# Kernel tuning notes

Measured on AMD Instinct MI355X. Metric: run time of the kernel, lower is better.

Reference implementation:

```python
import jax, jax.numpy as jnp
import numpy as np

IN_DIM, DIM, H, L, B, N = 20, 128, 8, 3, 2, 192
DH = DIM // H
EPS = 1e-5


def _conv1d(x, w):
    # x: [b, Cin, n], w: [Cout, Cin, 3], pad=1
    return jax.lax.conv_general_dilated(x, w, (1,), [(1, 1)], dimension_numbers=('NCH', 'OIH', 'NCH'))


def _conv2d(x, w):
    # x: [b, Cin, n, n], w: [Cout, Cin, 3, 3], pad=1
    return jax.lax.conv_general_dilated(x, w, (1, 1), [(1, 1), (1, 1)], dimension_numbers=('NCHW', 'OIHW', 'NCHW'))


def _bn(x, g, b, axes):
    # BatchNorm in training mode (batch statistics, biased variance), channel axis = 1
    m = jnp.mean(x, axes, keepdims=True)
    v = jnp.var(x, axes, keepdims=True)
    sh = [1] * x.ndim
    sh[1] = -1
    return (x - m) / jnp.sqrt(v + EPS) * g.reshape(sh) + b.reshape(sh)


def _ln(x, g, b):
    m = jnp.mean(x, -1, keepdims=True)
    v = jnp.var(x, -1, keepdims=True)
    return (x - m) / jnp.sqrt(v + EPS) * g + b


def _seq2pair(c):
    # c: [b, C, n] -> [b, 2C, n, n]; first C channels constant over j, second C constant over i
    b, C, n = c.shape
    a = jnp.broadcast_to(c[:, :, :, None], (b, C, n, n))
    p = jnp.broadcast_to(c[:, :, None, :], (b, C, n, n))
    return jnp.concatenate([a, p], axis=1)


def _forward(seq, mask, conv1_w, conv2_w, ln_g, ln_b, c1d_w, bn1_g, bn1_b, c2d_w, bn2_g, bn2_b,
             wq_w, wq_b, wk_w, wk_b, wv_w, wv_b, wd_w, wd_b, wl_w, wl_b, fc_w, fc_b):
    b, n, _ = seq.shape
    s = seq.transpose(0, 2, 1)                    # [b, in_dim, n]
    x = _conv1d(s, conv1_w).transpose(0, 2, 1)    # [b, n, dim]
    c = _conv1d(s, conv2_w)                       # [b, dim, n]
    c2 = _seq2pair(c)                             # [b, 2*dim, n, n]
    scale = jnp.sqrt(jnp.asarray(DH, x.dtype))
    m4 = mask[:, None, None, :]                   # [b, 1, 1, n]
    for i in range(L):
        c = jax.nn.relu(_bn(_conv1d(c, c1d_w[i]), bn1_g[i], bn1_b[i], (0, 2)))
        x = _ln(x + c.transpose(0, 2, 1), ln_g[i], ln_b[i])
        c2 = c2 + _seq2pair(c)
        c2 = jax.nn.relu(_bn(_conv2d(c2, c2d_w[i]), bn2_g[i], bn2_b[i], (0, 2, 3)))
        dsym = c2 + c2.transpose(0, 1, 3, 2)      # symmetric pair features [b, 2*dim, n, n]
        gate = jax.nn.sigmoid(jnp.einsum('bcij,hc->bhij', dsym, wd_w[i]) + wd_b[i][None, :, None, None])
        heads = lambda y: y.reshape(b, n, H, DH).transpose(0, 2, 1, 3)
        q = heads(jax.nn.relu(x @ wq_w[i].T + wq_b[i]))
        k = heads(jax.nn.relu(x @ wk_w[i].T + wk_b[i]))
        v = heads(jax.nn.relu(x @ wv_w[i].T + wv_b[i]))
        a = jnp.einsum('bhid,bhjd->bhij', q, k) / scale
        e = jnp.exp(a - jnp.max(a, -1, keepdims=True)) * m4   # hand-rolled masked softmax
        attn = e / (jnp.sum(e, -1, keepdims=True) + 1e-6)
        attn = attn * gate                        # post-softmax multiplicative pair bias
        upd = jnp.einsum('bhij,bhjd->bhid', attn, v).transpose(0, 2, 1, 3).reshape(b, n, DIM)
        x = jax.nn.relu((x + upd) @ wl_w[i].T + wl_b[i])   # dropout = identity (eval)
    return jax.nn.relu(x @ fc_w.T + fc_b)


def setup_inputs():
    key = jax.random.key(0)
    ks = jax.random.split(key, 16)
    rn = lambda k, shape, s=0.05: jax.random.normal(k, shape, jnp.float32) * s
    C2 = 2 * DIM
    return {
        'seq': jax.random.normal(ks[0], (B, N, IN_DIM), jnp.float32),
        'mask': (jax.random.uniform(ks[1], (B, N)) > 0.1).astype(jnp.float32),
        'conv1_w': rn(ks[2], (DIM, IN_DIM, 3)),
        'conv2_w': rn(ks[3], (DIM, IN_DIM, 3)),
        'ln_g': jnp.ones((L, DIM), jnp.float32),
        'ln_b': jnp.zeros((L, DIM), jnp.float32),
        'c1d_w': rn(ks[4], (L, DIM, DIM, 3)),
        'bn1_g': jnp.ones((L, DIM), jnp.float32),
        'bn1_b': jnp.zeros((L, DIM), jnp.float32),
        'c2d_w': rn(ks[5], (L, C2, C2, 3, 3), 0.02),
        'bn2_g': jnp.ones((L, C2), jnp.float32),
        'bn2_b': jnp.zeros((L, C2), jnp.float32),
        'wq_w': rn(ks[6], (L, DIM, DIM)), 'wq_b': jnp.zeros((L, DIM), jnp.float32),
        'wk_w': rn(ks[7], (L, DIM, DIM)), 'wk_b': jnp.zeros((L, DIM), jnp.float32),
        'wv_w': rn(ks[8], (L, DIM, DIM)), 'wv_b': jnp.zeros((L, DIM), jnp.float32),
        'wd_w': rn(ks[9], (L, H, C2)), 'wd_b': jnp.zeros((L, H), jnp.float32),
        'wl_w': rn(ks[10], (L, DIM, DIM)), 'wl_b': jnp.zeros((L, DIM), jnp.float32),
        'fc_w': rn(ks[11], (DIM, DIM)), 'fc_b': jnp.zeros((DIM,), jnp.float32),
    }


def reference(seq, mask, conv1_w, conv2_w, ln_g, ln_b, c1d_w, bn1_g, bn1_b, c2d_w, bn2_g, bn2_b,
              wq_w, wq_b, wk_w, wk_b, wv_w, wv_b, wd_w, wd_b, wl_w, wl_b, fc_w, fc_b):
    return _forward(seq, mask, conv1_w, conv2_w, ln_g, ln_b, c1d_w, bn1_g, bn1_b, c2d_w, bn2_g, bn2_b,
                    wq_w, wq_b, wk_w, wk_b, wv_w, wv_b, wd_w, wd_b, wl_w, wl_b, fc_w, fc_b)
```

## Files before the change

### kernel.cpp

```cpp
#include <hip/hip_runtime.h>
#include <math.h>

#define IN_DIM 20
#define DIM 128
#define HH 8
#define LL 3
#define BB 2
#define NP 192
#define DHH 16
#define C2 256
#define NN (NP*NP)
#define EPS 1e-5f

#define PR 200
#define PC 224

typedef __bf16 bf16x8 __attribute__((ext_vector_type(8)));
typedef float  f32x16 __attribute__((ext_vector_type(16)));

union Pack8 { __bf16 h[8]; uint4 u; };

#define GLOAD16(gp, lp) \
  __builtin_amdgcn_global_load_lds((const __attribute__((address_space(1))) uint4*)(gp), \
                                   (__attribute__((address_space(3))) uint4*)(lp), 16, 0, 0)

__global__ void k_conv_init(const float* __restrict__ seq, const float* __restrict__ w1,
                            const float* __restrict__ w2, float* __restrict__ X,
                            float* __restrict__ Cc) {
  int t = blockIdx.x, b = blockIdx.y, oc = threadIdx.x;
  __shared__ float ss[3][IN_DIM];
  if (threadIdx.x < 3*IN_DIM) {
    int k = threadIdx.x / IN_DIM, ic = threadIdx.x % IN_DIM;
    int tt = t + k - 1;
    ss[k][ic] = (tt >= 0 && tt < NP) ? seq[(b*NP + tt)*IN_DIM + ic] : 0.f;
  }
  __syncthreads();
  float a1 = 0.f, a2 = 0.f;
  #pragma unroll
  for (int ic = 0; ic < IN_DIM; ic++) {
    #pragma unroll
    for (int k = 0; k < 3; k++) {
      float sv = ss[k][ic];
      a1 = fmaf(w1[(oc*IN_DIM + ic)*3 + k], sv, a1);
      a2 = fmaf(w2[(oc*IN_DIM + ic)*3 + k], sv, a2);
    }
  }
  X[(b*NP + t)*DIM + oc] = a1;
  Cc[(b*DIM + oc)*NP + t] = a2;
}

__global__ __launch_bounds__(768)
void k_conv1d_bn_relu(const float* __restrict__ cin, const float* __restrict__ w,
                      const float* __restrict__ g, const float* __restrict__ bb,
                      float* __restrict__ cout) {
  int oc = blockIdx.x;
  int tid = threadIdx.x;
  int t = tid % NP;
  int sub = tid / NP;
  int b = sub & 1, ih = sub >> 1;
  float acc = 0.f;
  for (int ic = ih*64; ic < ih*64 + 64; ic++) {
    const float* cr = cin + (b*DIM + ic)*NP;
    const float* wr = w + (oc*DIM + ic)*3;
    float lf = (t > 0)      ? cr[t-1] : 0.f;
    float mf = cr[t];
    float rf = (t < NP-1)   ? cr[t+1] : 0.f;
    acc = fmaf(lf, wr[0], acc);
    acc = fmaf(mf, wr[1], acc);
    acc = fmaf(rf, wr[2], acc);
  }
  __shared__ float sp[4][NP];
  __shared__ float sb[768];
  sp[sub][t] = acc;
  __syncthreads();
  float raw = sp[b][t] + sp[2 + b][t];
  sb[tid] = (sub < 2) ? raw : raw * raw;
  __syncthreads();
  for (int s = 192; s >= 3; s >>= 1) {
    if (tid < s) sb[tid] += sb[tid + s];
    int u = tid - 384;
    if (u >= 0 && u < s) sb[tid] += sb[tid + s];
    __syncthreads();
  }
  float mean = (sb[0] + sb[1] + sb[2]) / 384.f;
  float var  = (sb[384] + sb[385] + sb[386]) / 384.f - mean*mean;
  float rstd = rsqrtf(var + EPS);
  if (sub < 2)
    cout[(b*DIM + oc)*NP + t] = fmaxf((raw - mean)*rstd*g[oc] + bb[oc], 0.f);
}

__global__ void k_wtrans(const float* __restrict__ wq, const float* __restrict__ wk,
                         const float* __restrict__ wv, const float* __restrict__ wl,
                         const float* __restrict__ fcw,
                         float* __restrict__ wqt, float* __restrict__ wkt,
                         float* __restrict__ wvt, float* __restrict__ wlt,
                         float* __restrict__ fct) {
  int m = blockIdx.y;
  const float* src; float* dst;
  if (m < 3)       { src = wq + (size_t)m*DIM*DIM;     dst = wqt + (size_t)m*DIM*DIM; }
  else if (m < 6)  { src = wk + (size_t)(m-3)*DIM*DIM; dst = wkt + (size_t)(m-3)*DIM*DIM; }
  else if (m < 9)  { src = wv + (size_t)(m-6)*DIM*DIM; dst = wvt + (size_t)(m-6)*DIM*DIM; }
  else if (m < 12) { src = wl + (size_t)(m-9)*DIM*DIM; dst = wlt + (size_t)(m-9)*DIM*DIM; }
  else             { src = fcw;                        dst = fct; }
  int tile = blockIdx.x;
  int ti = tile >> 2, tj = tile & 3;
  int r = threadIdx.x >> 3, c4 = threadIdx.x & 7;
  __shared__ float t[32][33];
  float4 v = *(const float4*)(src + (ti*32 + r)*DIM + tj*32 + c4*4);
  t[r][c4*4+0] = v.x; t[r][c4*4+1] = v.y; t[r][c4*4+2] = v.z; t[r][c4*4+3] = v.w;
  __syncthreads();
  float4 o;
  o.x = t[c4*4+0][r]; o.y = t[c4*4+1][r]; o.z = t[c4*4+2][r]; o.w = t[c4*4+3][r];
  *(float4*)(dst + (tj*32 + r)*DIM + ti*32 + c4*4) = o;
}

__global__ void k_lnqkv(float* __restrict__ X, const float* __restrict__ cc,
                        const float* __restrict__ g, const float* __restrict__ bb,
                        const float* __restrict__ wqt, const float* __restrict__ bq,
                        const float* __restrict__ wkt, const float* __restrict__ bk,
                        const float* __restrict__ wvt, const float* __restrict__ bv,
                        float* __restrict__ Q, float* __restrict__ K, float* __restrict__ V) {
  int t = blockIdx.x, b = blockIdx.y, d = threadIdx.x;
  __shared__ float sb[DIM];
  __shared__ float sy[DIM];
  float v = X[(b*NP + t)*DIM + d] + cc[(b*DIM + d)*NP + t];
  sb[d] = v; __syncthreads();
  for (int s = 64; s > 0; s >>= 1) { if (d < s) sb[d] += sb[d+s]; __syncthreads(); }
  float mean = sb[0] / (float)DIM;
  __syncthreads();
  float dv = v - mean;
  sb[d] = dv*dv; __syncthreads();
  for (int s = 64; s > 0; s >>= 1) { if (d < s) sb[d] += sb[d+s]; __syncthreads(); }
  float var = sb[0] / (float)DIM;
  float rstd = rsqrtf(var + EPS);
  float xn = dv * rstd * g[d] + bb[d];
  X[(b*NP + t)*DIM + d] = xn;
  sy[d] = xn;
  __syncthreads();
  float aq = bq[d], ak = bk[d], av = bv[d];
  for (int e = 0; e < DIM; e++) {
    float xv = sy[e];
    aq = fmaf(wqt[e*DIM + d], xv, aq);
    ak = fmaf(wkt[e*DIM + d], xv, ak);
    av = fmaf(wvt[e*DIM + d], xv, av);
  }
  int h = d >> 4, dh = d & 15;
  size_t o = ((size_t)(b*HH + h)*NP + t)*DHH + dh;
  Q[o] = fmaxf(aq, 0.f); K[o] = fmaxf(ak, 0.f); V[o] = fmaxf(av, 0.f);
}

__global__ void k_wprep(const float* __restrict__ w, __bf16* __restrict__ wtb) {
  int l = blockIdx.x / C2, oc = blockIdx.x % C2;
  int tid = threadIdx.x;
  __shared__ float swt[C2*9];
  const float4* wsrc = (const float4*)(w + ((size_t)(l*C2 + oc))*C2*9);
  for (int idx = tid; idx < 576; idx += 256) ((float4*)swt)[idx] = wsrc[idx];
  __syncthreads();
  for (int v = tid; v < 288; v += 256) {
    int chunk = v / 18, rem = v % 18;
    int kk = rem >> 1, kh = rem & 1;
    Pack8 p;
    #pragma unroll
    for (int e = 0; e < 8; e++)
      p.h[e] = (__bf16)swt[(chunk*16 + kh*8 + e)*9 + kk];
    size_t unit = ((((size_t)(l*16 + chunk)*9 + kk)*2 + kh)*256 + oc);
    ((uint4*)wtb)[unit] = p.u;
  }
}

__global__ void k_make_convin(const float* __restrict__ Cc, const float* __restrict__ CL0,
                              __bf16* __restrict__ inb, float* __restrict__ STATALL) {
  int idx = blockIdx.x*256 + threadIdx.x;
  if (blockIdx.x == 0) {
    for (int z = threadIdx.x; z < 3*2*C2; z += 256) STATALL[z] = 0.f;
  }
  int kh = idx & 1;
  int t = idx >> 1;
  int gcol = t % PC; int t2 = t / PC;
  int grow = t2 % PR; int t3 = t2 / PR;
  int chunk = t3 & 15; int b = t3 >> 4;
  int i = grow - 1, j = gcol - 8;
  Pack8 p;
  if ((unsigned)i < 192u && (unsigned)j < 192u) {
    #pragma unroll
    for (int e = 0; e < 8; e++) {
      int c = chunk*16 + kh*8 + e;
      float v;
      if (c < DIM) v = Cc[(b*DIM + c)*NP + i] + CL0[(b*DIM + c)*NP + i];
      else { int cc = c - DIM; v = Cc[(b*DIM + cc)*NP + j] + CL0[(b*DIM + cc)*NP + j]; }
      p.h[e] = (__bf16)v;
    }
  } else {
    #pragma unroll
    for (int e = 0; e < 8; e++) p.h[e] = (__bf16)0.f;
  }
  ((uint4*)inb)[idx] = p.u;
}

__global__ __launch_bounds__(256, 2)
void k_conv2d_mfma(const __bf16* __restrict__ inb,
                   const __bf16* __restrict__ wtb,
                   __bf16* __restrict__ rawb,
                   float* __restrict__ STAT2) {
  __shared__ __align__(16) uint4 sbuf[2*2176];
  int tid = threadIdx.x;
  int jt = blockIdx.x, it = blockIdx.y, zz = blockIdx.z;
  int b = zz >> 3, oct = zz & 7;
  int i0 = it*8, j0 = jt*64, oc0 = oct*32;
  int lane = tid & 63, wv = tid >> 6;
  int ln31 = lane & 31, khl = lane >> 5;

  const uint4* gW = (const uint4*)wtb;
  const uint4* gI = (const uint4*)inb;

  f32x16 acc[2][2];
  #pragma unroll
  for (int r = 0; r < 2; r++)
    #pragma unroll
    for (int n = 0; n < 2; n++)
      #pragma unroll
      for (int q = 0; q < 16; q++) acc[r][n][q] = 0.f;

  const uint4* gp[9];
  int lofs[9];
  int gstride[9];
  bool gvalid[9];
  #pragma unroll
  for (int t = 0; t < 9; t++) {
    int L = t*4 + wv;
    gvalid[t] = (L < 34);
    if (L < 9) {
      int u = L*64 + lane;
      int kkh = u >> 5;
      int ocl = u & 31;
      gp[t] = gW + (size_t)kkh*256 + oc0 + ocl;
      lofs[t] = u;
      gstride[t] = 4608;
    } else {
      int u = L*64 + lane - 576;
      int r = u / 160;
      int rem = u % 160;
      int kh = rem / 80;
      int c = rem % 80;
      gp[t] = gI + (((size_t)(b*16)*PR) + i0 + r)*PC*2 + (size_t)(j0 + c)*2 + kh;
      lofs[t] = 576 + u;
      gstride[t] = PR*PC*2;
    }
  }

  auto issue = [&](int buf) {
    uint4* lbase = sbuf + buf*2176;
    #pragma unroll
    for (int t = 0; t < 9; t++) {
      if (gvalid[t]) {
        GLOAD16(gp[t], lbase + lofs[t]);
        gp[t] += gstride[t];
      }
    }
  };

  issue(0);

  for (int chunk = 0; chunk < 16; ++chunk) {
    int buf = chunk & 1;
    __syncthreads();
    if (chunk < 15) issue(buf ^ 1);
    const __bf16* Wl = (const __bf16*)(sbuf + buf*2176);
    const __bf16* Il = (const __bf16*)(sbuf + buf*2176 + 576);
    #pragma unroll
    for (int kj = 0; kj < 3; kj++) {
      bf16x8 bfr[4][2];
      #pragma unroll
      for (int rr = 0; rr < 4; rr++) {
        int r = wv*2 + rr;
        #pragma unroll
        for (int ch = 0; ch < 2; ch++) {
          int c = ch*32 + ln31 + kj + 7;
          bfr[rr][ch] = *(const bf16x8*)(Il + ((r*2 + khl)*80 + c)*8);
        }
      }
      #pragma unroll
      for (int ki = 0; ki < 3; ki++) {
        int kk = ki*3 + kj;
        bf16x8 a = *(const bf16x8*)(Wl + ((kk*2 + khl)*32 + ln31)*8);
        #pragma unroll
        for (int row = 0; row < 2; row++)
          #pragma unroll
          for (int ch = 0; ch < 2; ch++)
            acc[row][ch] = __builtin_amdgcn_mfma_f32_32x32x16_bf16(a, bfr[row + ki][ch], acc[row][ch], 0, 0, 0);
      }
    }
  }

  __syncthreads();
  float* trAll = (float*)sbuf;
  float* tr = trAll + wv*(32*33);
  float* sstat = trAll + 4*32*33;
  if (tid < 64) sstat[tid] = 0.f;
  __syncthreads();

  #pragma unroll
  for (int reg = 0; reg < 16; reg++) {
    float v00 = acc[0][0][reg], v01 = acc[0][1][reg];
    float v10 = acc[1][0][reg], v11 = acc[1][1][reg];
    float s = v00 + v01 + v10 + v11;
    float s2 = v00*v00 + v01*v01 + v10*v10 + v11*v11;
    #pragma unroll
    for (int msk = 1; msk <= 16; msk <<= 1) { s += __shfl_xor(s, msk); s2 += __shfl_xor(s2, msk); }
    if (ln31 == 0) {
      int oc_l = (reg & 3) + 8*(reg >> 2) + 4*khl;
      atomicAdd(&sstat[oc_l], s);
      atomicAdd(&sstat[32 + oc_l], s2);
    }
  }

  int Gb = oc0 >> 3;
  uint4* RAWu = (uint4*)rawb;
  #pragma unroll
  for (int row = 0; row < 2; row++) {
    int i = i0 + wv*2 + row;
    #pragma unroll
    for (int ch = 0; ch < 2; ch++) {
      #pragma unroll
      for (int reg = 0; reg < 16; reg++) {
        int r = (reg & 3) + 8*(reg >> 2) + 4*khl;
        tr[r*33 + ln31] = acc[row][ch][reg];
      }
      __builtin_amdgcn_s_waitcnt(0);
      #pragma unroll
      for (int gs = 0; gs < 2; gs++) {
        int g = khl + gs*2;
        Pack8 p;
        #pragma unroll
        for (int e = 0; e < 8; e++) p.h[e] = (__bf16)tr[(g*8 + e)*33 + ln31];
        RAWu[((size_t)(b*32 + Gb + g)*192 + i)*192 + j0 + ch*32 + ln31] = p.u;
      }
      __builtin_amdgcn_s_waitcnt(0);
    }
  }

  __syncthreads();
  if (tid < 32) {
    atomicAdd(&STAT2[oc0 + tid], sstat[tid]);
    atomicAdd(&STAT2[C2 + oc0 + tid], sstat[32 + tid]);
  }
}

template<int WRITE_NEXT>
__global__ __launch_bounds__(384)
void k_bn2_norm_gate(const __bf16* __restrict__ rawb, const float* __restrict__ STAT2,
                     const float* __restrict__ g, const float* __restrict__ bb,
                     const float* __restrict__ wd, const float* __restrict__ CLn,
                     __bf16* __restrict__ inb_next, float* __restrict__ tg) {
  int i = blockIdx.x, b = blockIdx.y;
  int tid = threadIdx.x;
  int j = tid % 192, half = tid / 192;
  __shared__ float sscale[C2], sshift[C2], swd[HH*C2];
  __shared__ float sg[2][HH][192];
  const float inv = 1.f / (float)(BB*NN);
  for (int c = tid; c < C2; c += 384) {
    float mean = STAT2[c] * inv;
    float var  = STAT2[C2 + c] * inv - mean*mean;
    float rstd = rsqrtf(var + EPS);
    float sc = rstd * g[c];
    sscale[c] = sc;
    sshift[c] = bb[c] - mean*sc;
  }
  for (int idx = tid; idx < HH*C2; idx += 384) swd[idx] = wd[idx];
  __syncthreads();
  float gacc[HH] = {};
  const uint4* RAWu = (const uint4*)rawb;
  for (int cu = half*16; cu < half*16 + 16; cu++) {
    Pack8 pr; pr.u = RAWu[((size_t)(b*32 + cu)*NP + i)*NP + j];
    Pack8 p;
    #pragma unroll
    for (int e = 0; e < 8; e++) {
      int c = cu*8 + e;
      float v = (float)pr.h[e];
      v = fmaxf(fmaf(v, sscale[c], sshift[c]), 0.f);
      if (WRITE_NEXT) {
        float nv = v + ((c < DIM) ? CLn[(b*DIM + c)*NP + i] : CLn[(b*DIM + c - DIM)*NP + j]);
        p.h[e] = (__bf16)nv;
      }
      #pragma unroll
      for (int h = 0; h < HH; h++) gacc[h] = fmaf(v, swd[h*C2 + c], gacc[h]);
    }
    if (WRITE_NEXT) {
      size_t unit = ((((size_t)(b*16 + (cu>>1))*PR + (i+1))*PC + (j+8))*2 + (cu&1));
      ((uint4*)inb_next)[unit] = p.u;
    }
  }
  #pragma unroll
  for (int h = 0; h < HH; h++) sg[half][h][j] = gacc[h];
  __syncthreads();
  if (half == 0) {
    #pragma unroll
    for (int h = 0; h < HH; h++)
      tg[((size_t)(b*HH + h)*NP + i)*NP + j] = sg[0][h][j] + sg[1][h][j];
  }
}

__global__ void k_gate(const float* __restrict__ tg, const float* __restrict__ wdb,
                       float* __restrict__ gate) {
  int tile = blockIdx.x;
  int hb = blockIdx.y;
  int b = hb >> 3, h = hb & 7;
  size_t bh = (size_t)(b*HH + h);
  int ti = tile / 6, tj = tile % 6;
  int r = threadIdx.x >> 3, c4 = threadIdx.x & 7;
  __shared__ float tB[32][33];
  const float* base = tg + bh*NN;
  float4 vb = *(const float4*)(base + (tj*32 + r)*NP + ti*32 + c4*4);
  tB[r][c4*4+0] = vb.x; tB[r][c4*4+1] = vb.y; tB[r][c4*4+2] = vb.z; tB[r][c4*4+3] = vb.w;
  __syncthreads();
  float4 va = *(const float4*)(base + (ti*32 + r)*NP + tj*32 + c4*4);
  float bias = wdb[h];
  float4 o;
  o.x = 1.f / (1.f + expf(-(va.x + tB[c4*4+0][r] + bias)));
  o.y = 1.f / (1.f + expf(-(va.y + tB[c4*4+1][r] + bias)));
  o.z = 1.f / (1.f + expf(-(va.z + tB[c4*4+2][r] + bias)));
  o.w = 1.f / (1.f + expf(-(va.w + tB[c4*4+3][r] + bias)));
  *(float4*)(gate + bh*NN + (ti*32 + r)*NP + tj*32 + c4*4) = o;
}

template<int MODE>
__global__ __launch_bounds__(384)
void k_attnx(const float* __restrict__ Q, const float* __restrict__ K,
             const float* __restrict__ V, const float* __restrict__ gate,
             const float* __restrict__ mask,
             float* __restrict__ X,
             const float* __restrict__ wlt, const float* __restrict__ bl,
             const float* __restrict__ ccn,
             const float* __restrict__ lng, const float* __restrict__ lnb,
             const float* __restrict__ wqt, const float* __restrict__ bq,
             const float* __restrict__ wkt, const float* __restrict__ bk,
             const float* __restrict__ wvt, const float* __restrict__ bv,
             float* __restrict__ Qn, float* __restrict__ Kn, float* __restrict__ Vn,
             const float* __restrict__ fct, const float* __restrict__ fb,
             float* __restrict__ out) {
  int i = blockIdx.x, b = blockIdx.y;
  int tid = threadIdx.x;
  int j = tid % 192, half = tid / 192;
  int lane = tid & 63, wave = tid >> 6;
  __shared__ float sq[DIM];
  __shared__ float sattn[HH][NP];
  __shared__ float spv[3][DIM];
  __shared__ float supd[DIM];
  __shared__ float sy[DIM];
  __shared__ float sxp[3][DIM];
  __shared__ float sredm[HH][3];
  __shared__ float sreds[HH][3];
  __shared__ float sred[2];
  float mk = mask[b*NP + j];

  if (tid < DIM) {
    int h = tid >> 4, d = tid & 15;
    sq[tid] = Q[(((size_t)(b*HH + h))*NP + i)*DHH + d];
  }
  __syncthreads();

  float a[4], gt[4];
  #pragma unroll
  for (int hh = 0; hh < 4; hh++) {
    int h = half*4 + hh;
    size_t bh = (size_t)(b*HH + h);
    const float4* kr = (const float4*)(K + (bh*NP + j)*DHH);
    const float4* qr = (const float4*)(sq + h*DHH);
    float acc = 0.f;
    #pragma unroll
    for (int q4 = 0; q4 < 4; q4++) {
      float4 qv = qr[q4], kv = kr[q4];
      acc = fmaf(qv.x, kv.x, acc); acc = fmaf(qv.y, kv.y, acc);
      acc = fmaf(qv.z, kv.z, acc); acc = fmaf(qv.w, kv.w, acc);
    }
    a[hh] = acc * 0.25f;
    gt[hh] = gate[(bh*NP + i)*NP + j];
  }
  #pragma unroll
  for (int hh = 0; hh < 4; hh++) {
    int h = half*4 + hh;
    float m = a[hh];
    #pragma unroll
    for (int s = 32; s > 0; s >>= 1) m = fmaxf(m, __shfl_xor(m, s));
    if (lane == 0) sredm[h][wave % 3] = m;
  }
  __syncthreads();
  float e[4];
  #pragma unroll
  for (int hh = 0; hh < 4; hh++) {
    int h = half*4 + hh;
    float amax = fmaxf(fmaxf(sredm[h][0], sredm[h][1]), sredm[h][2]);
    e[hh] = expf(a[hh] - amax) * mk;
    float ss = e[hh];
    #pragma unroll
    for (int s = 32; s > 0; s >>= 1) ss += __shfl_xor(ss, s);
    if (lane == 0) sreds[h][wave % 3] = ss;
  }
  __syncthreads();
  #pragma unroll
  for (int hh = 0; hh < 4; hh++) {
    int h = half*4 + hh;
    float denom = sreds[h][0] + sreds[h][1] + sreds[h][2] + 1e-6f;
    sattn[h][j] = (e[hh] / denom) * gt[hh];
  }
  __syncthreads();

  {
    int d = tid & 15, h2 = (tid >> 4) & 7, jseg = tid >> 7;
    size_t bh = (size_t)(b*HH + h2);
    float acc = 0.f;
    for (int jj = jseg*64; jj < jseg*64 + 64; jj++)
      acc = fmaf(sattn[h2][jj], V[(bh*NP + jj)*DHH + d], acc);
    spv[jseg][h2*DHH + d] = acc;
  }
  __syncthreads();
  if (tid < DIM) supd[tid] = spv[0][tid] + spv[1][tid] + spv[2][tid];
  __syncthreads();

  size_t o = (size_t)(b*NP + i)*DIM;
  if (tid < DIM) sy[tid] = X[o + tid] + supd[tid];
  __syncthreads();
  {
    int d2 = tid & 127, ks = tid >> 7;
    int e0 = ks*43, e1 = (ks == 2) ? 128 : e0 + 43;
    float acc = (ks == 0) ? bl[d2] : 0.f;
    for (int ee = e0; ee < e1; ee++) acc = fmaf(wlt[ee*DIM + d2], sy[ee], acc);
    sxp[ks][d2] = acc;
  }
  __syncthreads();
  float xr = 0.f;
  if (tid < DIM) xr = fmaxf(sxp[0][tid] + sxp[1][tid] + sxp[2][tid], 0.f);
  __syncthreads();

  if (MODE == 0) {
    float v = 0.f;
    if (tid < DIM) v = xr + ccn[(b*DIM + tid)*NP + i];
    if (tid < DIM) {
      float s = v;
      #pragma unroll
      for (int m = 32; m > 0; m >>= 1) s += __shfl_xor(s, m);
      if (lane == 0) sred[wave] = s;
    }
    __syncthreads();
    float mean = (sred[0] + sred[1]) * (1.f/128.f);
    float dv = v - mean;
    if (tid < DIM) {
      float q = dv*dv;
      #pragma unroll
      for (int m = 32; m > 0; m >>= 1) q += __shfl_xor(q, m);
      if (lane == 0) sred[wave] = q;
    }
    __syncthreads();
    float var = (sred[0] + sred[1]) * (1.f/128.f);
    float rstd = rsqrtf(var + EPS);
    if (tid < DIM) {
      float xn = dv * rstd * lng[tid] + lnb[tid];
      X[o + tid] = xn;
      sy[tid] = xn;
    }
    __syncthreads();
    {
      int d2 = tid & 127, m = tid >> 7;
      const float* wt_m = (m == 0) ? wqt : (m == 1) ? wkt : wvt;
      const float* b_m  = (m == 0) ? bq  : (m == 1) ? bk  : bv;
      float* out_m      = (m == 0) ? Qn  : (m == 1) ? Kn  : Vn;
      float acc = b_m[d2];
      for (int ee = 0; ee < DIM; ee++) acc = fmaf(wt_m[ee*DIM + d2], sy[ee], acc);
      int h = d2 >> 4, dh = d2 & 15;
      out_m[((size_t)(b*HH + h)*NP + i)*DHH + dh] = fmaxf(acc, 0.f);
    }
  } else {
    if (tid < DIM) sy[tid] = xr;
    __syncthreads();
    {
      int d2 = tid & 127, ks = tid >> 7;
      int e0 = ks*43, e1 = (ks == 2) ? 128 : e0 + 43;
      float acc = (ks == 0) ? fb[d2] : 0.f;
      for (int ee = e0; ee < e1; ee++) acc = fmaf(fct[ee*DIM + d2], sy[ee], acc);
      sxp[ks][d2] = acc;
    }
    __syncthreads();
    if (tid < DIM)
      out[o + tid] = fmaxf(sxp[0][tid] + sxp[1][tid] + sxp[2][tid], 0.f);
  }
}

extern "C" void kernel_launch(void* const* d_in, const int* in_sizes, int n_in,
                              void* d_out, int out_size, void* d_ws, size_t ws_size,
                              hipStream_t stream) {
  const float* seq     = (const float*)d_in[0];
  const float* mask    = (const float*)d_in[1];
  const float* conv1_w = (const float*)d_in[2];
  const float* conv2_w = (const float*)d_in[3];
  const float* ln_g    = (const float*)d_in[4];
  const float* ln_b    = (const float*)d_in[5];
  const float* c1d_w   = (const float*)d_in[6];
  const float* bn1_g   = (const float*)d_in[7];
  const float* bn1_b   = (const float*)d_in[8];
  const float* c2d_w   = (const float*)d_in[9];
  const float* bn2_g   = (const float*)d_in[10];
  const float* bn2_b   = (const float*)d_in[11];
  const float* wq_w    = (const float*)d_in[12];
  const float* wq_b    = (const float*)d_in[13];
  const float* wk_w    = (const float*)d_in[14];
  const float* wk_b    = (const float*)d_in[15];
  const float* wv_w    = (const float*)d_in[16];
  const float* wv_b    = (const float*)d_in[17];
  const float* wd_w    = (const float*)d_in[18];
  const float* wd_b    = (const float*)d_in[19];
  const float* wl_w    = (const float*)d_in[20];
  const float* wl_b    = (const float*)d_in[21];
  const float* fc_w    = (const float*)d_in[22];
  const float* fc_b    = (const float*)d_in[23];
  float* out = (float*)d_out;

  float* ws = (float*)d_ws;
  float* X    = ws; ws += BB*NP*DIM;
  float* Cc   = ws; ws += BB*DIM*NP;
  float* CL0  = ws; ws += BB*DIM*NP;
  float* CL1  = ws; ws += BB*DIM*NP;
  float* CL2  = ws; ws += BB*DIM*NP;
  float* Q0   = ws; ws += BB*NP*DIM;
  float* K0   = ws; ws += BB*NP*DIM;
  float* V0   = ws; ws += BB*NP*DIM;
  float* Q1   = ws; ws += BB*NP*DIM;
  float* K1   = ws; ws += BB*NP*DIM;
  float* V1   = ws; ws += BB*NP*DIM;
  float* TG   = ws; ws += (size_t)BB*HH*NN;
  float* GATE = ws; ws += (size_t)BB*HH*NN;
  float* WQT  = ws; ws += (size_t)LL*DIM*DIM;
  float* WKT  = ws; ws += (size_t)LL*DIM*DIM;
  float* WVT  = ws; ws += (size_t)LL*DIM*DIM;
  float* WLT  = ws; ws += (size_t)LL*DIM*DIM;
  float* FCT  = ws; ws += (size_t)DIM*DIM;
  float* STATALL = ws; ws += 3*2*C2;
  __bf16* RAW = (__bf16*)ws; ws += (size_t)BB*C2*NN/2;
  __bf16* INB = (__bf16*)ws; ws += (size_t)BB*16*PR*PC*2*16/4;
  __bf16* WTB = (__bf16*)ws; ws += (size_t)LL*C2*C2*9/2;

  k_wtrans<<<dim3(16, 13), 256, 0, stream>>>(wq_w, wk_w, wv_w, wl_w, fc_w,
                                             WQT, WKT, WVT, WLT, FCT);
  k_wprep<<<LL*C2, 256, 0, stream>>>(c2d_w, WTB);
  k_conv_init<<<dim3(NP, BB), DIM, 0, stream>>>(seq, conv1_w, conv2_w, X, Cc);
  k_conv1d_bn_relu<<<DIM, 768, 0, stream>>>(Cc,  c1d_w + 0*(size_t)DIM*DIM*3, bn1_g + 0*DIM, bn1_b + 0*DIM, CL0);
  k_conv1d_bn_relu<<<DIM, 768, 0, stream>>>(CL0, c1d_w + 1*(size_t)DIM*DIM*3, bn1_g + 1*DIM, bn1_b + 1*DIM, CL1);
  k_conv1d_bn_relu<<<DIM, 768, 0, stream>>>(CL1, c1d_w + 2*(size_t)DIM*DIM*3, bn1_g + 2*DIM, bn1_b + 2*DIM, CL2);
  k_make_convin<<<(BB*16*PR*PC*2)/256, 256, 0, stream>>>(Cc, CL0, INB, STATALL);
  k_lnqkv<<<dim3(NP, BB), DIM, 0, stream>>>(X, CL0, ln_g, ln_b,
                                            WQT, wq_b, WKT, wk_b, WVT, wv_b, Q0, K0, V0);

  k_conv2d_mfma<<<dim3(3, 24, 16), 256, 0, stream>>>(INB, WTB + 0*(size_t)16*9*2*256*8, RAW, STATALL + 0*2*C2);
  k_bn2_norm_gate<1><<<dim3(NP, BB), 384, 0, stream>>>(RAW, STATALL + 0*2*C2, bn2_g + 0*C2, bn2_b + 0*C2,
                                                       wd_w + 0*(size_t)HH*C2, CL1, INB, TG);
  k_gate<<<dim3(36, 16), 256, 0, stream>>>(TG, wd_b + 0*HH, GATE);
  k_attnx<0><<<dim3(NP, BB), 384, 0, stream>>>(Q0, K0, V0, GATE, mask, X,
                                               WLT + 0*(size_t)DIM*DIM, wl_b + 0*DIM,
                                               CL1, ln_g + 1*DIM, ln_b + 1*DIM,
                                               WQT + 1*(size_t)DIM*DIM, wq_b + 1*DIM,
                                               WKT + 1*(size_t)DIM*DIM, wk_b + 1*DIM,
                                               WVT + 1*(size_t)DIM*DIM, wv_b + 1*DIM,
                                               Q1, K1, V1, nullptr, nullptr, nullptr);
  k_conv2d_mfma<<<dim3(3, 24, 16), 256, 0, stream>>>(INB, WTB + 1*(size_t)16*9*2*256*8, RAW, STATALL + 1*2*C2);
  k_bn2_norm_gate<1><<<dim3(NP, BB), 384, 0, stream>>>(RAW, STATALL + 1*2*C2, bn2_g + 1*C2, bn2_b + 1*C2,
                                                       wd_w + 1*(size_t)HH*C2, CL2, INB, TG);
  k_gate<<<dim3(36, 16), 256, 0, stream>>>(TG, wd_b + 1*HH, GATE);
  k_attnx<0><<<dim3(NP, BB), 384, 0, stream>>>(Q1, K1, V1, GATE, mask, X,
                                               WLT + 1*(size_t)DIM*DIM, wl_b + 1*DIM,
                                               CL2, ln_g + 2*DIM, ln_b + 2*DIM,
                                               WQT + 2*(size_t)DIM*DIM, wq_b + 2*DIM,
                                               WKT + 2*(size_t)DIM*DIM, wk_b + 2*DIM,
                                               WVT + 2*(size_t)DIM*DIM, wv_b + 2*DIM,
                                               Q0, K0, V0, nullptr, nullptr, nullptr);
  k_conv2d_mfma<<<dim3(3, 24, 16), 256, 0, stream>>>(INB, WTB + 2*(size_t)16*9*2*256*8, RAW, STATALL + 2*2*C2);
  k_bn2_norm_gate<0><<<dim3(NP, BB), 384, 0, stream>>>(RAW, STATALL + 2*2*C2, bn2_g + 2*C2, bn2_b + 2*C2,
                                                       wd_w + 2*(size_t)HH*C2, nullptr, nullptr, TG);
  k_gate<<<dim3(36, 16), 256, 0, stream>>>(TG, wd_b + 2*HH, GATE);
  k_attnx<1><<<dim3(NP, BB), 384, 0, stream>>>(Q0, K0, V0, GATE, mask, X,
                                               WLT + 2*(size_t)DIM*DIM, wl_b + 2*DIM,
                                               nullptr, nullptr, nullptr,
                                               nullptr, nullptr, nullptr, nullptr, nullptr, nullptr,
                                               nullptr, nullptr, nullptr,
                                               FCT, fc_b, out);
}
```

Measured before the change: 591.5 us.

## Add position-major copies of 1D conv features and widen BN2/LNQKV blocks

The 1D conv kernels now also write a transposed [b, n, dim] copy of their output. Consumers (make_convin, bn2_norm_gate, lnqkv, attnx) read contiguous channel runs from that copy instead of strided per-channel loads. bn2_norm_gate moves from 384 to 768 threads, each quarter handling 8 channel units. lnqkv uses wave shuffles and splits the Q/K/V projections across 384 threads. This costs extra workspace and extra writes, in exchange for fewer scattered reads and more parallelism per block.

```diff
diff --git a/kernel.cpp b/kernel.cpp
--- a/kernel.cpp
+++ b/kernel.cpp
@@ -26,7 +26,7 @@
 
 __global__ void k_conv_init(const float* __restrict__ seq, const float* __restrict__ w1,
                             const float* __restrict__ w2, float* __restrict__ X,
-                            float* __restrict__ Cc) {
+                            float* __restrict__ Cc, float* __restrict__ CcT) {
   int t = blockIdx.x, b = blockIdx.y, oc = threadIdx.x;
   __shared__ float ss[3][IN_DIM];
   if (threadIdx.x < 3*IN_DIM) {
@@ -47,12 +47,13 @@
   }
   X[(b*NP + t)*DIM + oc] = a1;
   Cc[(b*DIM + oc)*NP + t] = a2;
+  CcT[(size_t)(b*NP + t)*DIM + oc] = a2;
 }
 
 __global__ __launch_bounds__(768)
 void k_conv1d_bn_relu(const float* __restrict__ cin, const float* __restrict__ w,
                       const float* __restrict__ g, const float* __restrict__ bb,
-                      float* __restrict__ cout) {
+                      float* __restrict__ cout, float* __restrict__ coutT) {
   int oc = blockIdx.x;
   int tid = threadIdx.x;
   int t = tid % NP;
@@ -85,8 +86,11 @@
   float mean = (sb[0] + sb[1] + sb[2]) / 384.f;
   float var  = (sb[384] + sb[385] + sb[386]) / 384.f - mean*mean;
   float rstd = rsqrtf(var + EPS);
-  if (sub < 2)
-    cout[(b*DIM + oc)*NP + t] = fmaxf((raw - mean)*rstd*g[oc] + bb[oc], 0.f);
+  if (sub < 2) {
+    float v = fmaxf((raw - mean)*rstd*g[oc] + bb[oc], 0.f);
+    cout[(b*DIM + oc)*NP + t] = v;
+    coutT[(size_t)(b*NP + t)*DIM + oc] = v;
+  }
 }
 
 __global__ void k_wtrans(const float* __restrict__ wq, const float* __restrict__ wk,
@@ -114,39 +118,56 @@
   *(float4*)(dst + (tj*32 + r)*DIM + ti*32 + c4*4) = o;
 }
 
-__global__ void k_lnqkv(float* __restrict__ X, const float* __restrict__ cc,
-                        const float* __restrict__ g, const float* __restrict__ bb,
-                        const float* __restrict__ wqt, const float* __restrict__ bq,
-                        const float* __restrict__ wkt, const float* __restrict__ bk,
-                        const float* __restrict__ wvt, const float* __restrict__ bv,
-                        float* __restrict__ Q, float* __restrict__ K, float* __restrict__ V) {
-  int t = blockIdx.x, b = blockIdx.y, d = threadIdx.x;
-  __shared__ float sb[DIM];
+__global__ __launch_bounds__(384)
+void k_lnqkv(float* __restrict__ X, const float* __restrict__ ccT,
+             const float* __restrict__ g, const float* __restrict__ bb,
+             const float* __restrict__ wqt, const float* __restrict__ bq,
+             const float* __restrict__ wkt, const float* __restrict__ bk,
+             const float* __restrict__ wvt, const float* __restrict__ bv,
+             float* __restrict__ Q, float* __restrict__ K, float* __restrict__ V) {
+  int t = blockIdx.x, b = blockIdx.y;
+  int tid = threadIdx.x;
+  int lane = tid & 63, wave = tid >> 6;
   __shared__ float sy[DIM];
-  float v = X[(b*NP + t)*DIM + d] + cc[(b*DIM + d)*NP + t];
-  sb[d] = v; __syncthreads();
-  for (int s = 64; s > 0; s >>= 1) { if (d < s) sb[d] += sb[d+s]; __syncthreads(); }
-  float mean = sb[0] / (float)DIM;
-  __syncthreads();
+  __shared__ float sred[2];
+  size_t o = (size_t)(b*NP + t)*DIM;
+  float v = 0.f;
+  if (tid < DIM) v = X[o + tid] + ccT[o + tid];
+  if (tid < DIM) {
+    float s = v;
+    #pragma unroll
+    for (int m = 32; m > 0; m >>= 1) s += __shfl_xor(s, m);
+    if (lane == 0) sred[wave] = s;
+  }
+  __syncthreads();
+  float mean = (sred[0] + sred[1]) * (1.f/128.f);
   float dv = v - mean;
-  sb[d] = dv*dv; __syncthreads();
-  for (int s = 64; s > 0; s >>= 1) { if (d < s) sb[d] += sb[d+s]; __syncthreads(); }
-  float var = sb[0] / (float)DIM;
+  __syncthreads();
+  if (tid < DIM) {
+    float q = dv*dv;
+    #pragma unroll
+    for (int m = 32; m > 0; m >>= 1) q += __shfl_xor(q, m);
+    if (lane == 0) sred[wave] = q;
+  }
+  __syncthreads();
+  float var = (sred[0] + sred[1]) * (1.f/128.f);
   float rstd = rsqrtf(var + EPS);
-  float xn = dv * rstd * g[d] + bb[d];
-  X[(b*NP + t)*DIM + d] = xn;
-  sy[d] = xn;
-  __syncthreads();
-  float aq = bq[d], ak = bk[d], av = bv[d];
-  for (int e = 0; e < DIM; e++) {
-    float xv = sy[e];
-    aq = fmaf(wqt[e*DIM + d], xv, aq);
-    ak = fmaf(wkt[e*DIM + d], xv, ak);
-    av = fmaf(wvt[e*DIM + d], xv, av);
-  }
-  int h = d >> 4, dh = d & 15;
-  size_t o = ((size_t)(b*HH + h)*NP + t)*DHH + dh;
-  Q[o] = fmaxf(aq, 0.f); K[o] = fmaxf(ak, 0.f); V[o] = fmaxf(av, 0.f);
+  if (tid < DIM) {
+    float xn = dv * rstd * g[tid] + bb[tid];
+    X[o + tid] = xn;
+    sy[tid] = xn;
+  }
+  __syncthreads();
+  {
+    int d2 = tid & 127, m = tid >> 7;
+    const float* wt_m = (m == 0) ? wqt : (m == 1) ? wkt : wvt;
+    const float* b_m  = (m == 0) ? bq  : (m == 1) ? bk  : bv;
+    float* out_m      = (m == 0) ? Q   : (m == 1) ? K   : V;
+    float acc = b_m[d2];
+    for (int ee = 0; ee < DIM; ee++) acc = fmaf(wt_m[ee*DIM + d2], sy[ee], acc);
+    int h = d2 >> 4, dh = d2 & 15;
+    out_m[((size_t)(b*HH + h)*NP + t)*DHH + dh] = fmaxf(acc, 0.f);
+  }
 }
 
 __global__ void k_wprep(const float* __restrict__ w, __bf16* __restrict__ wtb) {
@@ -168,7 +189,7 @@
   }
 }
 
-__global__ void k_make_convin(const float* __restrict__ Cc, const float* __restrict__ CL0,
+__global__ void k_make_convin(const float* __restrict__ CcT, const float* __restrict__ CLT0,
                               __bf16* __restrict__ inb, float* __restrict__ STATALL) {
   int idx = blockIdx.x*256 + threadIdx.x;
   if (blockIdx.x == 0) {
@@ -182,14 +203,18 @@
   int i = grow - 1, j = gcol - 8;
   Pack8 p;
   if ((unsigned)i < 192u && (unsigned)j < 192u) {
-    #pragma unroll
-    for (int e = 0; e < 8; e++) {
-      int c = chunk*16 + kh*8 + e;
-      float v;
-      if (c < DIM) v = Cc[(b*DIM + c)*NP + i] + CL0[(b*DIM + c)*NP + i];
-      else { int cc = c - DIM; v = Cc[(b*DIM + cc)*NP + j] + CL0[(b*DIM + cc)*NP + j]; }
-      p.h[e] = (__bf16)v;
-    }
+    int cbase = chunk*16 + kh*8;
+    const float* pa;
+    const float* pb;
+    if (cbase < DIM) {
+      pa = CcT  + (size_t)(b*NP + i)*DIM + cbase;
+      pb = CLT0 + (size_t)(b*NP + i)*DIM + cbase;
+    } else {
+      pa = CcT  + (size_t)(b*NP + j)*DIM + (cbase - DIM);
+      pb = CLT0 + (size_t)(b*NP + j)*DIM + (cbase - DIM);
+    }
+    #pragma unroll
+    for (int e = 0; e < 8; e++) p.h[e] = (__bf16)(pa[e] + pb[e]);
   } else {
     #pragma unroll
     for (int e = 0; e < 8; e++) p.h[e] = (__bf16)0.f;
@@ -347,18 +372,18 @@
 }
 
 template<int WRITE_NEXT>
-__global__ __launch_bounds__(384)
+__global__ __launch_bounds__(768)
 void k_bn2_norm_gate(const __bf16* __restrict__ rawb, const float* __restrict__ STAT2,
                      const float* __restrict__ g, const float* __restrict__ bb,
-                     const float* __restrict__ wd, const float* __restrict__ CLn,
+                     const float* __restrict__ wd, const float* __restrict__ CLnT,
                      __bf16* __restrict__ inb_next, float* __restrict__ tg) {
   int i = blockIdx.x, b = blockIdx.y;
   int tid = threadIdx.x;
-  int j = tid % 192, half = tid / 192;
+  int j = tid % 192, qt = tid / 192;
   __shared__ float sscale[C2], sshift[C2], swd[HH*C2];
-  __shared__ float sg[2][HH][192];
+  __shared__ float sg[4][HH][192];
   const float inv = 1.f / (float)(BB*NN);
-  for (int c = tid; c < C2; c += 384) {
+  for (int c = tid; c < C2; c += 768) {
     float mean = STAT2[c] * inv;
     float var  = STAT2[C2 + c] * inv - mean*mean;
     float rstd = rsqrtf(var + EPS);
@@ -366,22 +391,24 @@
     sscale[c] = sc;
     sshift[c] = bb[c] - mean*sc;
   }
-  for (int idx = tid; idx < HH*C2; idx += 384) swd[idx] = wd[idx];
+  for (int idx = tid; idx < HH*C2; idx += 768) swd[idx] = wd[idx];
   __syncthreads();
   float gacc[HH] = {};
   const uint4* RAWu = (const uint4*)rawb;
-  for (int cu = half*16; cu < half*16 + 16; cu++) {
+  const float* clrow_i = CLnT ? CLnT + (size_t)(b*NP + i)*DIM : nullptr;
+  const float* clrow_j = CLnT ? CLnT + (size_t)(b*NP + j)*DIM : nullptr;
+  for (int cu = qt*8; cu < qt*8 + 8; cu++) {
     Pack8 pr; pr.u = RAWu[((size_t)(b*32 + cu)*NP + i)*NP + j];
     Pack8 p;
+    int cbase = cu*8;
+    const float* clp = (WRITE_NEXT && cbase < DIM) ? clrow_i + cbase
+                     : (WRITE_NEXT ? clrow_j + (cbase - DIM) : nullptr);
     #pragma unroll
     for (int e = 0; e < 8; e++) {
-      int c = cu*8 + e;
+      int c = cbase + e;
       float v = (float)pr.h[e];
       v = fmaxf(fmaf(v, sscale[c], sshift[c]), 0.f);
-      if (WRITE_NEXT) {
-        float nv = v + ((c < DIM) ? CLn[(b*DIM + c)*NP + i] : CLn[(b*DIM + c - DIM)*NP + j]);
-        p.h[e] = (__bf16)nv;
-      }
+      if (WRITE_NEXT) p.h[e] = (__bf16)(v + clp[e]);
       #pragma unroll
       for (int h = 0; h < HH; h++) gacc[h] = fmaf(v, swd[h*C2 + c], gacc[h]);
     }
@@ -391,12 +418,12 @@
     }
   }
   #pragma unroll
-  for (int h = 0; h < HH; h++) sg[half][h][j] = gacc[h];
-  __syncthreads();
-  if (half == 0) {
+  for (int h = 0; h < HH; h++) sg[qt][h][j] = gacc[h];
+  __syncthreads();
+  if (qt == 0) {
     #pragma unroll
     for (int h = 0; h < HH; h++)
-      tg[((size_t)(b*HH + h)*NP + i)*NP + j] = sg[0][h][j] + sg[1][h][j];
+      tg[((size_t)(b*HH + h)*NP + i)*NP + j] = sg[0][h][j] + sg[1][h][j] + sg[2][h][j] + sg[3][h][j];
   }
 }
 
@@ -430,7 +457,7 @@
              const float* __restrict__ mask,
              float* __restrict__ X,
              const float* __restrict__ wlt, const float* __restrict__ bl,
-             const float* __restrict__ ccn,
+             const float* __restrict__ ccnT,
              const float* __restrict__ lng, const float* __restrict__ lnb,
              const float* __restrict__ wqt, const float* __restrict__ bq,
              const float* __restrict__ wkt, const float* __restrict__ bk,
@@ -534,7 +561,7 @@
 
   if (MODE == 0) {
     float v = 0.f;
-    if (tid < DIM) v = xr + ccn[(b*DIM + tid)*NP + i];
+    if (tid < DIM) v = xr + ccnT[o + tid];
     if (tid < DIM) {
       float s = v;
       #pragma unroll
@@ -544,6 +571,7 @@
     __syncthreads();
     float mean = (sred[0] + sred[1]) * (1.f/128.f);
     float dv = v - mean;
+    __syncthreads();
     if (tid < DIM) {
       float q = dv*dv;
       #pragma unroll
@@ -617,9 +645,13 @@
   float* ws = (float*)d_ws;
   float* X    = ws; ws += BB*NP*DIM;
   float* Cc   = ws; ws += BB*DIM*NP;
+  float* CcT  = ws; ws += BB*DIM*NP;
   float* CL0  = ws; ws += BB*DIM*NP;
   float* CL1  = ws; ws += BB*DIM*NP;
   float* CL2  = ws; ws += BB*DIM*NP;
+  float* CLT0 = ws; ws += BB*DIM*NP;
+  float* CLT1 = ws; ws += BB*DIM*NP;
+  float* CLT2 = ws; ws += BB*DIM*NP;
   float* Q0   = ws; ws += BB*NP*DIM;
   float* K0   = ws; ws += BB*NP*DIM;
   float* V0   = ws; ws += BB*NP*DIM;
@@ -641,38 +673,38 @@
   k_wtrans<<<dim3(16, 13), 256, 0, stream>>>(wq_w, wk_w, wv_w, wl_w, fc_w,
                                              WQT, WKT, WVT, WLT, FCT);
   k_wprep<<<LL*C2, 256, 0, stream>>>(c2d_w, WTB);
-  k_conv_init<<<dim3(NP, BB), DIM, 0, stream>>>(seq, conv1_w, conv2_w, X, Cc);
-  k_conv1d_bn_relu<<<DIM, 768, 0, stream>>>(Cc,  c1d_w + 0*(size_t)DIM*DIM*3, bn1_g + 0*DIM, bn1_b + 0*DIM, CL0);
-  k_conv1d_bn_relu<<<DIM, 768, 0, stream>>>(CL0, c1d_w + 1*(size_t)DIM*DIM*3, bn1_g + 1*DIM, bn1_b + 1*DIM, CL1);
-  k_conv1d_bn_relu<<<DIM, 768, 0, stream>>>(CL1, c1d_w + 2*(size_t)DIM*DIM*3, bn1_g + 2*DIM, bn1_b + 2*DIM, CL2);
-  k_make_convin<<<(BB*16*PR*PC*2)/256, 256, 0, stream>>>(Cc, CL0, INB, STATALL);
-  k_lnqkv<<<dim3(NP, BB), DIM, 0, stream>>>(X, CL0, ln_g, ln_b,
+  k_conv_init<<<dim3(NP, BB), DIM, 0, stream>>>(seq, conv1_w, conv2_w, X, Cc, CcT);
+  k_conv1d_bn_relu<<<DIM, 768, 0, stream>>>(Cc,  c1d_w + 0*(size_t)DIM*DIM*3, bn1_g + 0*DIM, bn1_b + 0*DIM, CL0, CLT0);
+  k_conv1d_bn_relu<<<DIM, 768, 0, stream>>>(CL0, c1d_w + 1*(size_t)DIM*DIM*3, bn1_g + 1*DIM, bn1_b + 1*DIM, CL1, CLT1);
+  k_conv1d_bn_relu<<<DIM, 768, 0, stream>>>(CL1, c1d_w + 2*(size_t)DIM*DIM*3, bn1_g + 2*DIM, bn1_b + 2*DIM, CL2, CLT2);
+  k_make_convin<<<(BB*16*PR*PC*2)/256, 256, 0, stream>>>(CcT, CLT0, INB, STATALL);
+  k_lnqkv<<<dim3(NP, BB), 384, 0, stream>>>(X, CLT0, ln_g, ln_b,
                                             WQT, wq_b, WKT, wk_b, WVT, wv_b, Q0, K0, V0);
 
   k_conv2d_mfma<<<dim3(3, 24, 16), 256, 0, stream>>>(INB, WTB + 0*(size_t)16*9*2*256*8, RAW, STATALL + 0*2*C2);
-  k_bn2_norm_gate<1><<<dim3(NP, BB), 384, 0, stream>>>(RAW, STATALL + 0*2*C2, bn2_g + 0*C2, bn2_b + 0*C2,
-                                                       wd_w + 0*(size_t)HH*C2, CL1, INB, TG);
+  k_bn2_norm_gate<1><<<dim3(NP, BB), 768, 0, stream>>>(RAW, STATALL + 0*2*C2, bn2_g + 0*C2, bn2_b + 0*C2,
+                                                       wd_w + 0*(size_t)HH*C2, CLT1, INB, TG);
   k_gate<<<dim3(36, 16), 256, 0, stream>>>(TG, wd_b + 0*HH, GATE);
   k_attnx<0><<<dim3(NP, BB), 384, 0, stream>>>(Q0, K0, V0, GATE, mask, X,
                                                WLT + 0*(size_t)DIM*DIM, wl_b + 0*DIM,
-                                               CL1, ln_g + 1*DIM, ln_b + 1*DIM,
+                                               CLT1, ln_g + 1*DIM, ln_b + 1*DIM,
                                                WQT + 1*(size_t)DIM*DIM, wq_b + 1*DIM,
                                                WKT + 1*(size_t)DIM*DIM, wk_b + 1*DIM,
                                                WVT + 1*(size_t)DIM*DIM, wv_b + 1*DIM,
                                                Q1, K1, V1, nullptr, nullptr, nullptr);
   k_conv2d_mfma<<<dim3(3, 24, 16), 256, 0, stream>>>(INB, WTB + 1*(size_t)16*9*2*256*8, RAW, STATALL + 1*2*C2);
-  k_bn2_norm_gate<1><<<dim3(NP, BB), 384, 0, stream>>>(RAW, STATALL + 1*2*C2, bn2_g + 1*C2, bn2_b + 1*C2,
-                                                       wd_w + 1*(size_t)HH*C2, CL2, INB, TG);
+  k_bn2_norm_gate<1><<<dim3(NP, BB), 768, 0, stream>>>(RAW, STATALL + 1*2*C2, bn2_g + 1*C2, bn2_b + 1*C2,
+                                                       wd_w + 1*(size_t)HH*C2, CLT2, INB, TG);
   k_gate<<<dim3(36, 16), 256, 0, stream>>>(TG, wd_b + 1*HH, GATE);
   k_attnx<0><<<dim3(NP, BB), 384, 0, stream>>>(Q1, K1, V1, GATE, mask, X,
                                                WLT + 1*(size_t)DIM*DIM, wl_b + 1*DIM,
-                                               CL2, ln_g + 2*DIM, ln_b + 2*DIM,
+                                               CLT2, ln_g + 2*DIM, ln_b + 2*DIM,
                                                WQT + 2*(size_t)DIM*DIM, wq_b + 2*DIM,
                                                WKT + 2*(size_t)DIM*DIM, wk_b + 2*DIM,
                                                WVT + 2*(size_t)DIM*DIM, wv_b + 2*DIM,
                                                Q0, K0, V0, nullptr, nullptr, nullptr);
   k_conv2d_mfma<<<dim3(3, 24, 16), 256, 0, stream>>>(INB, WTB + 2*(size_t)16*9*2*256*8, RAW, STATALL + 2*2*C2);
-  k_bn2_norm_gate<0><<<dim3(NP, BB), 384, 0, stream>>>(RAW, STATALL + 2*2*C2, bn2_g + 2*C2, bn2_b + 2*C2,
+  k_bn2_norm_gate<0><<<dim3(NP, BB), 768, 0, stream>>>(RAW, STATALL + 2*2*C2, bn2_g + 2*C2, bn2_b + 2*C2,
                                                        wd_w + 2*(size_t)HH*C2, nullptr, nullptr, TG);
   k_gate<<<dim3(36, 16), 256, 0, stream>>>(TG, wd_b + 2*HH, GATE);
   k_attnx<1><<<dim3(NP, BB), 384, 0, stream>>>(Q0, K0, V0, GATE, mask, X,
```

Result: faster. 575.7 us (median of 2 runs) (-2.7%).
